# Optimization experiments

Measured on AMD Instinct MI355X. Metric: run time of the kernel, lower is better.

Reference implementation:

```python
import jax, jax.numpy as jnp
import numpy as np

SPIN_LEN = 365
TRAIN_LEN = 200000
ML = 2.9086  # mean of second forcing (hard-coded in the torch module)
SL = 1.898   # std of second forcing (hard-coded in the torch module)


def setup_inputs() -> dict:
    key = jax.random.key(0)
    kx, ky, kp = jax.random.split(key, 3)
    B, S = 262144, 1
    x = jax.random.uniform(kx, (B, S, 2), dtype=jnp.float32)
    y_obs = jax.random.uniform(ky, (B, 1), dtype=jnp.float32)
    ks = jax.random.split(kp, 6)
    return {
        "x": x,
        "y_obs": y_obs,
        "epoch": 1,
        "time_lag": 0,
        "weight_r_yom": jax.random.uniform(ks[0], (1, 1), dtype=jnp.float32),
        "weight_r_yom_gw": jax.random.uniform(ks[1], (1, 1), dtype=jnp.float32),
        "weight_r_ylm": jax.random.uniform(ks[2], (1, 1), dtype=jnp.float32),
        "weight_r_yfm": jax.random.uniform(ks[3], (1, 1), dtype=jnp.float32),
        "bias_b0_ylm": jax.random.uniform(ks[4], (1,), dtype=jnp.float32),
        "weight_b2_ylm": jax.random.uniform(ks[5], (1, 1), dtype=jnp.float32),
    }


def reference(x, y_obs, epoch, time_lag, weight_r_yom, weight_r_yom_gw,
              weight_r_ylm, weight_r_yfm, bias_b0_ylm, weight_b2_ylm):
    # x: [B, S, 2] (batch_first). The torch code transposes to [S, B, 2] and
    # runs b-outer / t-inner loops with state threaded across BOTH loops, so
    # the scan order over flattened steps is b-major, t-minor.
    B, S, _ = x.shape
    dt = x.dtype

    # softmax-like mass-balance gate normalization over the 4 scalar weights
    e_om = jnp.exp(weight_r_yom[0, 0])
    e_gw = jnp.exp(weight_r_yom_gw[0, 0])
    e_lm = jnp.exp(weight_r_ylm[0, 0])
    e_fm = jnp.exp(weight_r_yfm[0, 0])
    denom = e_om + e_gw + e_lm + e_fm
    oo = e_om / denom      # constant output gate
    oogw = e_gw / denom    # constant groundwater gate
    ol1 = e_lm / denom     # loss-gate scale
    b0 = bias_b0_ylm[0]
    wb2 = weight_b2_ylm[0, 0]

    # unbiased std, matching torch.std default
    obsstd = jnp.std(y_obs[SPIN_LEN:TRAIN_LEN], ddof=1)

    xv = x[time_lag:]                       # [B', S, 2] (time_lag is static)
    Bp = B - time_lag
    u1 = xv[..., 0].reshape(-1)             # [B'*S] inflow
    u2 = xv[..., 1].reshape(-1)             # [B'*S] loss forcing

    def step(c, u):
        u1_t, u2_t = u
        ol = ol1 * jax.nn.sigmoid(b0 + (u2_t - ML) / SL * wb2)
        f = 1.0 - oo - ol - oogw
        c_new = f * c + u1_t                # ib = 0 -> full inflow enters
        return c_new, (c, ol, f)

    _, (c_prev, ol_s, f_s) = jax.lax.scan(step, jnp.zeros((), dt), (u1, u2))

    # torch stores outputs every t but overwrites; only last t per b survives,
    # using c_0 (state BEFORE that step) and that step's ol/f.
    c0 = c_prev.reshape(Bp, S)[:, -1]
    olL = ol_s.reshape(Bp, S)[:, -1]
    fL = f_s.reshape(Bp, S)[:, -1]

    def pad(v):  # rows b < time_lag stay zero, shape [B, 1]
        return jnp.pad(v, (time_lag, 0))[:, None]

    h_n = pad(oo * c0)          # bp = 0 so h_n == q_n
    c_n = pad(c0)
    l_n = pad(olL * c0)
    gw_n = pad(oogw * c0)
    bp_n = jnp.zeros((B, 1), dt)
    gate_ib = jnp.zeros((B, 1), dt)
    valid = pad(jnp.ones((Bp,), dt))
    gate_oo = oo * valid
    gate_oogw = oogw * valid
    gate_ol = pad(olL)
    gate_f = pad(fL)
    obs_std = obsstd * valid
    h_nout = jnp.concatenate([h_n, obs_std], axis=1)
    return (h_n, c_n, l_n, gw_n, bp_n, gate_ib, gate_oo, gate_oogw,
            gate_ol, gate_f, h_nout, obs_std)
```

## Files before the change

### kernel.cpp

```cpp
#include <hip/hip_runtime.h>
#include <math.h>

#define SPIN 365
#define TRAINL 200000
#define ML 2.9086f
#define SLINV (1.0f / 1.898f)

#define THREADS 256
#define ITEMS 2
#define CHUNK (THREADS * ITEMS)
#define NW (THREADS / 64)

typedef float v2f __attribute__((ext_vector_type(2)));
typedef float v4f __attribute__((ext_vector_type(4)));

struct Sc { float oo, oogw, ol1, b0, k; };

__device__ __forceinline__ Sc get_sc(const float* w0, const float* w1,
                                     const float* w2, const float* w3,
                                     const float* b0p, const float* wb2p) {
  float e_om = __expf(w0[0]);
  float e_gw = __expf(w1[0]);
  float e_lm = __expf(w2[0]);
  float e_fm = __expf(w3[0]);
  float denom = e_om + e_gw + e_lm + e_fm;
  Sc s;
  s.oo   = e_om / denom;
  s.oogw = e_gw / denom;
  s.ol1  = e_lm / denom;
  s.b0   = b0p[0];
  s.k    = wb2p[0] * SLINV;
  return s;
}

__device__ __forceinline__ float sigm_fast(float z) {
  return __fdividef(1.0f, 1.0f + __expf(-z));
}

__device__ __forceinline__ void nts2(float* p, float a, float b) {
  v2f v = { a, b };
  __builtin_nontemporal_store(v, (v2f*)p);
}
__device__ __forceinline__ void nts4(float* p, float a, float b, float c, float d) {
  v4f v = { a, b, c, d };
  __builtin_nontemporal_store(v, (v4f*)p);
}


extern "C" __global__ __launch_bounds__(THREADS) void k1(
    const float* __restrict__ x, const float* __restrict__ y,
    const int* __restrict__ tlp,
    const float* __restrict__ w0, const float* __restrict__ w1,
    const float* __restrict__ w2, const float* __restrict__ w3,
    const float* __restrict__ b0p, const float* __restrict__ wb2p,
    float* __restrict__ out, float* __restrict__ ws, int B, int G)
{
  const int g = blockIdx.x, tid = threadIdx.x;
  const int lane = tid & 63, wid = tid >> 6;
  const int tl = tlp[0];
  const Sc sc = get_sc(w0, w1, w2, w3, b0p, wb2p);
  const int base = g * CHUNK + tid * ITEMS;
  const bool full = (base + ITEMS) <= B;

  float u1v[ITEMS], u2v[ITEMS];
  if (full) {
    float4 a = *(const float4*)(x + 2 * (size_t)base);
    u1v[0] = a.x; u2v[0] = a.y; u1v[1] = a.z; u2v[1] = a.w;
  } else {
    for (int j = 0; j < ITEMS; j++) {
      int p = base + j;
      u1v[j] = (p < B) ? x[2*(size_t)p]     : 0.f;
      u2v[j] = (p < B) ? x[2*(size_t)p + 1] : 0.f;
    }
  }

  float P = 1.f, Q = 0.f;
  float olv[ITEMS], fv[ITEMS];
  for (int j = 0; j < ITEMS; j++) {
    int p = base + j;
    float ol = sc.ol1 * sigm_fast(sc.b0 + (u2v[j] - ML) * sc.k);
    float f  = 1.0f - sc.oo - ol - sc.oogw;
    olv[j] = ol; fv[j] = f;
    bool act = (p >= tl) && (p < B);
    if (act) { Q = f * Q + u1v[j]; P *= f; }
  }

  if (full) {
    bool a0 = (base >= tl), a1 = (base + 1 >= tl);
    nts2(out + 4*(size_t)B + base, 0.f, 0.f);
    nts2(out + 5*(size_t)B + base, 0.f, 0.f);
    nts2(out + 6*(size_t)B + base, a0?sc.oo:0.f,   a1?sc.oo:0.f);
    nts2(out + 7*(size_t)B + base, a0?sc.oogw:0.f, a1?sc.oogw:0.f);
    nts2(out + 8*(size_t)B + base, a0?olv[0]:0.f,  a1?olv[1]:0.f);
    nts2(out + 9*(size_t)B + base, a0?fv[0]:0.f,   a1?fv[1]:0.f);
  } else {
    for (int j = 0; j < ITEMS; j++) {
      int p = base + j;
      if (p < B) {
        bool act = (p >= tl);
        out[4*(size_t)B+p] = 0.f;                  out[5*(size_t)B+p] = 0.f;
        out[6*(size_t)B+p] = act ? sc.oo   : 0.f;  out[7*(size_t)B+p] = act ? sc.oogw : 0.f;
        out[8*(size_t)B+p] = act ? olv[j]  : 0.f;  out[9*(size_t)B+p] = act ? fv[j]   : 0.f;
      }
    }
  }

  #pragma unroll
  for (int off = 1; off < 64; off <<= 1) {
    float pL = __shfl_down(P, off);
    float qL = __shfl_down(Q, off);
    Q = pL * Q + qL;
    P = pL * P;
  }

  float s = 0.f, ss = 0.f;
  if (full && base < TRAINL) {
    float2 yv = *(const float2*)(y + base);
    float vv[2] = { yv.x, yv.y };
    for (int j = 0; j < ITEMS; j++) {
      int p = base + j;
      if (p >= SPIN && p < TRAINL) { s += vv[j]; ss += vv[j]*vv[j]; }
    }
  } else {
    for (int j = 0; j < ITEMS; j++) {
      int p = base + j;
      if (p >= SPIN && p < TRAINL && p < B) { float v = y[p]; s += v; ss += v*v; }
    }
  }
  #pragma unroll
  for (int off = 1; off < 64; off <<= 1) {
    s  += __shfl_xor(s,  off);
    ss += __shfl_xor(ss, off);
  }

  __shared__ float wA[NW], wB[NW], rS[NW], rSS[NW];
  if (lane == 0) { wA[wid] = P; wB[wid] = Q; rS[wid] = s; rSS[wid] = ss; }
  __syncthreads();
  if (tid == 0) {
    float A = 1.f, Bq = 0.f, S = 0.f, SS = 0.f;
    #pragma unroll
    for (int w = 0; w < NW; w++) {
      Bq = wA[w] * Bq + wB[w];
      A  = wA[w] * A;
      S += rS[w]; SS += rSS[w];
    }
    ws[g] = A; ws[G + g] = Bq; ws[2*G + g] = S; ws[3*G + g] = SS;
  }
}

extern "C" __global__ __launch_bounds__(THREADS) void k2(
    const float* __restrict__ x, const int* __restrict__ tlp,
    const float* __restrict__ w0, const float* __restrict__ w1,
    const float* __restrict__ w2, const float* __restrict__ w3,
    const float* __restrict__ b0p, const float* __restrict__ wb2p,
    float* __restrict__ out, const float* __restrict__ ws, int B, int G)
{
  const int g = blockIdx.x, tid = threadIdx.x;
  const int lane = tid & 63, wid = tid >> 6;
  const int tl = tlp[0];
  const int YB = min(G, (TRAINL + CHUNK - 1) / CHUNK);
  const Sc sc = get_sc(w0, w1, w2, w3, b0p, wb2p);
  const int base = g * CHUNK + tid * ITEMS;
  const bool full = (base + ITEMS) <= B;

  const int i0 = 2 * tid, i1 = 2 * tid + 1;
  float aP0 = (i0 < G) ? ws[i0]     : 1.f;
  float aQ0 = (i0 < G) ? ws[G + i0] : 0.f;
  float aP1 = (i1 < G) ? ws[i1]     : 1.f;
  float aQ1 = (i1 < G) ? ws[G + i1] : 0.f;
  float yS  = ((tid)       < YB) ? ws[2*G + tid]       : 0.f;
  float ySS = ((tid)       < YB) ? ws[3*G + tid]       : 0.f;
  if (tid + THREADS < YB) { yS += ws[2*G + THREADS + tid]; ySS += ws[3*G + THREADS + tid]; }

  float u1v[ITEMS], u2v[ITEMS];
  if (full) {
    float4 a = *(const float4*)(x + 2 * (size_t)base);
    u1v[0] = a.x; u2v[0] = a.y; u1v[1] = a.z; u2v[1] = a.w;
  } else {
    for (int j = 0; j < ITEMS; j++) {
      int p = base + j;
      u1v[j] = (p < B) ? x[2*(size_t)p]     : 0.f;
      u2v[j] = (p < B) ? x[2*(size_t)p + 1] : 0.f;
    }
  }
  float P = 1.f, Q = 0.f;
  float olv[ITEMS], fv[ITEMS];
  for (int j = 0; j < ITEMS; j++) {
    int p = base + j;
    float ol = sc.ol1 * sigm_fast(sc.b0 + (u2v[j] - ML) * sc.k);
    float f  = 1.0f - sc.oo - ol - sc.oogw;
    olv[j] = ol; fv[j] = f;
    bool act = (p >= tl) && (p < B);
    if (act) { Q = f * Q + u1v[j]; P *= f; }
  }

  float iP = P, iQ = Q;
  #pragma unroll
  for (int off = 1; off < 64; off <<= 1) {
    float pa = __shfl_up(iP, off);
    float pb = __shfl_up(iQ, off);
    if (lane >= off) { iQ = iP * pb + iQ; iP = iP * pa; }
  }

  float cP = aP1 * aP0;
  float cQ = aP1 * aQ0 + aQ1;
  float jP = cP, jQ = cQ;
  #pragma unroll
  for (int off = 1; off < 64; off <<= 1) {
    float pa = __shfl_up(jP, off);
    float pb = __shfl_up(jQ, off);
    if (lane >= off) { jQ = jP * pb + jQ; jP = jP * pa; }
  }

  #pragma unroll
  for (int off = 1; off < 64; off <<= 1) {
    yS  += __shfl_xor(yS,  off);
    ySS += __shfl_xor(ySS, off);
  }

  __shared__ float wOA[NW], wOB[NW];
  __shared__ float wAA[NW], wAB[NW];
  __shared__ float rS[NW], rSS[NW];
  __shared__ float sQ[2 * THREADS];
  if (lane == 63) { wOA[wid] = iP; wOB[wid] = iQ; wAA[wid] = jP; wAB[wid] = jQ; }
  if (lane == 0)  { rS[wid] = yS; rSS[wid] = ySS; }
  __syncthreads();

  float OWA = 1.f, OWB = 0.f, AWA = 1.f, AWB = 0.f;
  for (int w = 0; w < wid; w++) {
    OWB = wOA[w] * OWB + wOB[w];  OWA *= wOA[w];
    AWB = wAA[w] * AWB + wAB[w];  AWA *= wAA[w];
  }

  float pe = __shfl_up(jP, 1);
  float qe = __shfl_up(jQ, 1);
  if (lane == 0) { pe = 1.f; qe = 0.f; }
  float EQ = pe * AWB + qe;
  float incQ0 = aP0 * EQ + aQ0;
  float incQ1 = aP1 * incQ0 + aQ1;
  sQ[i0] = incQ0;
  if (i1 < 2 * THREADS) sQ[i1] = incQ1;

  float S = 0.f, SS = 0.f;
  #pragma unroll
  for (int w = 0; w < NW; w++) { S += rS[w]; SS += rSS[w]; }
  float nY = (float)(TRAINL - SPIN);
  float mean = S / nY;
  float var = (SS - nY * mean * mean) / (nY - 1.0f);
  float ostd = sqrtf(fmaxf(var, 0.f));
  __syncthreads();

  const float Cg = (g == 0) ? 0.f : sQ[g - 1];

  float eP = __shfl_up(iP, 1);
  float eQ = __shfl_up(iQ, 1);
  if (lane == 0) { eP = 1.f; eQ = 0.f; }
  const float Ae = eP * OWA;
  const float Be = eP * OWB + eQ;

  float c = Ae * Cg + Be;
  float vh[ITEMS], vc[ITEMS], vl[ITEMS], vgw[ITEMS], vos[ITEMS];
  for (int j = 0; j < ITEMS; j++) {
    int p = base + j;
    bool act = (p >= tl) && (p < B);
    float c0 = c;
    vh[j]  = sc.oo * c0;
    vc[j]  = c0;
    vl[j]  = olv[j] * c0;
    vgw[j] = sc.oogw * c0;
    vos[j] = act ? ostd : 0.f;
    if (act) { c = fv[j] * c + u1v[j]; }
  }

  if (full) {
    nts2(out + (size_t)base,        vh[0],  vh[1]);
    nts2(out + (size_t)B + base,    vc[0],  vc[1]);
    nts2(out + 2*(size_t)B + base,  vl[0],  vl[1]);
    nts2(out + 3*(size_t)B + base,  vgw[0], vgw[1]);
    nts2(out + 12*(size_t)B + base, vos[0], vos[1]);
    nts4(out + 10*(size_t)B + 2*(size_t)base, vh[0], vos[0], vh[1], vos[1]);
  } else {
    for (int j = 0; j < ITEMS; j++) {
      int p = base + j;
      if (p < B) {
        out[(size_t)p]            = vh[j];
        out[(size_t)B + p]        = vc[j];
        out[2*(size_t)B + p]      = vl[j];
        out[3*(size_t)B + p]      = vgw[j];
        out[12*(size_t)B + p]     = vos[j];
        out[10*(size_t)B + 2*p]     = vh[j];
        out[10*(size_t)B + 2*p + 1] = vos[j];
      }
    }
  }
}

extern "C" void kernel_launch(void* const* d_in, const int* in_sizes, int n_in,
                              void* d_out, int out_size, void* d_ws, size_t ws_size,
                              hipStream_t stream) {
  const float* x   = (const float*)d_in[0];
  const float* y   = (const float*)d_in[1];
  const int*   tl  = (const int*)d_in[3];
  const float* w0  = (const float*)d_in[4];
  const float* w1  = (const float*)d_in[5];
  const float* w2  = (const float*)d_in[6];
  const float* w3  = (const float*)d_in[7];
  const float* b0  = (const float*)d_in[8];
  const float* wb2 = (const float*)d_in[9];

  float* out = (float*)d_out;
  float* ws  = (float*)d_ws;

  const int B = in_sizes[0] / 2;
  const int G = (B + CHUNK - 1) / CHUNK;

  k1<<<G, THREADS, 0, stream>>>(x, y, tl, w0, w1, w2, w3, b0, wb2, out, ws, B, G);
  k2<<<G, THREADS, 0, stream>>>(x, tl, w0, w1, w2, w3, b0, wb2, out, ws, B, G);
}
```

Measured before the change: 81.68 us.

## Double block size and split warps between carry scan and y-stat reduction

Block size goes from 256 to 512 threads, so each block covers twice as many elements and there are half as many blocks (G becomes 256). In the second kernel, the first four warps now scan the per-block carries with one carry per thread, and the other four warps sum the y-statistics partials, replacing the old scheme where every thread handled two carries and also reduced stats. The first kernel's y load becomes a nontemporal load. The new code hardcodes 4 warps and 256 carries, so it silently depends on G ≤ 256 and YB ≤ 256.

```diff
diff --git a/kernel.cpp b/kernel.cpp
--- a/kernel.cpp
+++ b/kernel.cpp
@@ -6,7 +6,7 @@
 #define ML 2.9086f
 #define SLINV (1.0f / 1.898f)
 
-#define THREADS 256
+#define THREADS 512
 #define ITEMS 2
 #define CHUNK (THREADS * ITEMS)
 #define NW (THREADS / 64)
@@ -115,7 +115,7 @@
 
   float s = 0.f, ss = 0.f;
   if (full && base < TRAINL) {
-    float2 yv = *(const float2*)(y + base);
+    v2f yv = __builtin_nontemporal_load((const v2f*)(y + base));
     float vv[2] = { yv.x, yv.y };
     for (int j = 0; j < ITEMS; j++) {
       int p = base + j;
@@ -163,14 +163,14 @@
   const int base = g * CHUNK + tid * ITEMS;
   const bool full = (base + ITEMS) <= B;
 
-  const int i0 = 2 * tid, i1 = 2 * tid + 1;
-  float aP0 = (i0 < G) ? ws[i0]     : 1.f;
-  float aQ0 = (i0 < G) ? ws[G + i0] : 0.f;
-  float aP1 = (i1 < G) ? ws[i1]     : 1.f;
-  float aQ1 = (i1 < G) ? ws[G + i1] : 0.f;
-  float yS  = ((tid)       < YB) ? ws[2*G + tid]       : 0.f;
-  float ySS = ((tid)       < YB) ? ws[3*G + tid]       : 0.f;
-  if (tid + THREADS < YB) { yS += ws[2*G + THREADS + tid]; ySS += ws[3*G + THREADS + tid]; }
+  float aP = 1.f, aQ = 0.f, yS = 0.f, ySS = 0.f;
+  if (tid < G) {
+    aP = ws[tid];
+    aQ = ws[G + tid];
+  } else {
+    int k = tid - G;
+    if (k < YB) { yS = ws[2*G + k]; ySS = ws[3*G + k]; }
+  }
 
   float u1v[ITEMS], u2v[ITEMS];
   if (full) {
@@ -202,16 +202,13 @@
     if (lane >= off) { iQ = iP * pb + iQ; iP = iP * pa; }
   }
 
-  float cP = aP1 * aP0;
-  float cQ = aP1 * aQ0 + aQ1;
-  float jP = cP, jQ = cQ;
+  float jP = aP, jQ = aQ;
   #pragma unroll
   for (int off = 1; off < 64; off <<= 1) {
     float pa = __shfl_up(jP, off);
     float pb = __shfl_up(jQ, off);
     if (lane >= off) { jQ = jP * pb + jQ; jP = jP * pa; }
   }
-
   #pragma unroll
   for (int off = 1; off < 64; off <<= 1) {
     yS  += __shfl_xor(yS,  off);
@@ -219,31 +216,27 @@
   }
 
   __shared__ float wOA[NW], wOB[NW];
-  __shared__ float wAA[NW], wAB[NW];
-  __shared__ float rS[NW], rSS[NW];
-  __shared__ float sQ[2 * THREADS];
-  if (lane == 63) { wOA[wid] = iP; wOB[wid] = iQ; wAA[wid] = jP; wAB[wid] = jQ; }
-  if (lane == 0)  { rS[wid] = yS; rSS[wid] = ySS; }
+  __shared__ float wAA[4], wAB[4];
+  __shared__ float rS[4], rSS[4];
+  __shared__ float sQ[256];
+  if (lane == 63) {
+    wOA[wid] = iP; wOB[wid] = iQ;
+    if (wid < 4) { wAA[wid] = jP; wAB[wid] = jQ; }
+  }
+  if (lane == 0 && wid >= 4) { rS[wid - 4] = yS; rSS[wid - 4] = ySS; }
   __syncthreads();
 
-  float OWA = 1.f, OWB = 0.f, AWA = 1.f, AWB = 0.f;
-  for (int w = 0; w < wid; w++) {
-    OWB = wOA[w] * OWB + wOB[w];  OWA *= wOA[w];
-    AWB = wAA[w] * AWB + wAB[w];  AWA *= wAA[w];
-  }
-
-  float pe = __shfl_up(jP, 1);
-  float qe = __shfl_up(jQ, 1);
-  if (lane == 0) { pe = 1.f; qe = 0.f; }
-  float EQ = pe * AWB + qe;
-  float incQ0 = aP0 * EQ + aQ0;
-  float incQ1 = aP1 * incQ0 + aQ1;
-  sQ[i0] = incQ0;
-  if (i1 < 2 * THREADS) sQ[i1] = incQ1;
-
-  float S = 0.f, SS = 0.f;
-  #pragma unroll
-  for (int w = 0; w < NW; w++) { S += rS[w]; SS += rSS[w]; }
+  float OWA = 1.f, OWB = 0.f;
+  for (int w = 0; w < wid; w++) { OWB = wOA[w] * OWB + wOB[w]; OWA *= wOA[w]; }
+
+  if (tid < G) {
+    float AWB = 0.f, AWA = 1.f;
+    for (int w = 0; w < wid; w++) { AWB = wAA[w] * AWB + wAB[w]; AWA *= wAA[w]; }
+    sQ[tid] = jP * AWB + jQ;
+  }
+
+  float S = rS[0] + rS[1] + rS[2] + rS[3];
+  float SS = rSS[0] + rSS[1] + rSS[2] + rSS[3];
   float nY = (float)(TRAINL - SPIN);
   float mean = S / nY;
   float var = (SS - nY * mean * mean) / (nY - 1.0f);
```

Result: no change. 80.92 us (-0.9%).
